# Optimization experiments

Measured on AMD Instinct MI355X. Metric: run time of the kernel, lower is better.

## Reference

```python
import jax, jax.numpy as jnp
import numpy as np

B, S, DIN, H, DOUT, E, SEL = 8, 2048, 512, 512, 512, 262144, 512
N = B * S


def setup_inputs() -> dict:
    key = jax.random.key(0)
    ks = jax.random.split(key, 20)
    inp = {
        "x": jax.random.normal(ks[0], (B, S, DIN), dtype=jnp.float32),
        "edge_index": jax.random.randint(ks[1], (2, E), 0, N, dtype=jnp.int64),
        "selected_idx": jax.random.randint(ks[2], (B, SEL), 0, S, dtype=jnp.int64),
        "edge_label": jax.random.randint(ks[3], (E,), 0, 8, dtype=jnp.int64),
    }
    k = 4
    for l, fin in enumerate([DIN, H, H]):
        inp[f"conv{l}_w1"] = jax.random.normal(ks[k], (2 * fin, H), dtype=jnp.float32) * 0.02; k += 1
        inp[f"conv{l}_b1"] = jnp.full((H,), 0.01, dtype=jnp.float32)
        inp[f"conv{l}_w2"] = jax.random.normal(ks[k], (H, H), dtype=jnp.float32) * 0.02; k += 1
        inp[f"conv{l}_b2"] = jnp.full((H,), 0.01, dtype=jnp.float32)
    inp["ffn_w1"] = jax.random.normal(ks[k], (H, H), dtype=jnp.float32) * 0.02; k += 1
    inp["ffn_b1"] = jnp.full((H,), 0.01, dtype=jnp.float32)
    inp["ffn_w2"] = jax.random.normal(ks[k], (H, DOUT), dtype=jnp.float32) * 0.02; k += 1
    inp["ffn_b2"] = jnp.full((DOUT,), 0.01, dtype=jnp.float32)
    return inp


def _ffw(x, w1, b1, w2, b2):
    # FeedForward: fc2(act_dropout(relu(fc1(x)))), dropout=0 in eval
    return jax.nn.relu(x @ w1 + b1) @ w2 + b2


def reference(x, edge_index, selected_idx, edge_label,
              conv0_w1, conv0_b1, conv0_w2, conv0_b2,
              conv1_w1, conv1_b1, conv1_w2, conv1_b2,
              conv2_w1, conv2_b1, conv2_w2, conv2_b2,
              ffn_w1, ffn_b1, ffn_w2, ffn_b2):
    b, s, d = x.shape
    n = b * s
    h = x.reshape(n, d)
    src, dst = edge_index[0], edge_index[1]  # PyG: x_j = source, x_i = target
    convs = [(conv0_w1, conv0_b1, conv0_w2, conv0_b2),
             (conv1_w1, conv1_b1, conv1_w2, conv1_b2),
             (conv2_w1, conv2_b1, conv2_w2, conv2_b2)]
    for w1, b1, w2, b2 in convs:
        xi = h[dst]                                   # [E, F]
        xj = h[src]
        ef = jnp.concatenate([xi, xj - xi], axis=1)   # [E, 2F]
        m = _ffw(ef, w1, b1, w2, b2)                  # per-edge MLP [E, H]
        agg = jax.ops.segment_max(m, dst, num_segments=n)
        agg = jnp.where(jnp.isneginf(agg), 0.0, agg)  # empty segments -> 0 (PyG fill)
        h = jax.nn.relu(agg)                          # dropout p acts as identity in eval
    h = _ffw(h, ffn_w1, ffn_b1, ffn_w2, ffn_b2)
    out = h.reshape(b, s, -1)                         # [B, S, DOUT]
    idx = jnp.broadcast_to(selected_idx[:, :, None], (b, selected_idx.shape[1], out.shape[-1]))
    return jnp.take_along_axis(out, idx, axis=1)      # [B, SEL, DOUT]
```

## Files before the change

### kernel.cpp

```cpp
#include <hip/hip_runtime.h>
#include <hip/hip_bf16.h>


#define N_NODES 16384
#define EDGES   262144
#define HDIM    512
#define SEQ     2048

typedef __attribute__((ext_vector_type(8))) short short8;
typedef __attribute__((ext_vector_type(8))) _Float16 half8;
typedef __attribute__((ext_vector_type(2))) _Float16 half2v;
typedef __attribute__((ext_vector_type(4))) float f32x4;

__device__ __forceinline__ void gld16(const void* g, void* l) {
    __builtin_amdgcn_global_load_lds(
        (const __attribute__((address_space(1))) void*)g,
        (__attribute__((address_space(3))) void*)l, 16, 0, 0);
}
__device__ __forceinline__ unsigned short f2b(float f) {
    unsigned int x = __float_as_uint(f);
    return (unsigned short)((x + 0x7fffu + ((x >> 16) & 1u)) >> 16);
}
__device__ __forceinline__ unsigned short f2h(float f) {
    _Float16 h = (_Float16)f;
    return __builtin_bit_cast(unsigned short, h);
}
__device__ __forceinline__ unsigned int zpack_h(unsigned int u, unsigned int v) {
    half2v a = __builtin_bit_cast(half2v, u);
    half2v b = __builtin_bit_cast(half2v, v);
    half2v s = a + b;
    half2v z = {(_Float16)0.f, (_Float16)0.f};
    half2v r = __builtin_elementwise_max(s, z);
    return __builtin_bit_cast(unsigned int, r);
}
__device__ __forceinline__ short8 frag_ld(const short* S, int row, int q) {
    int p = q ^ ((row >> 1) & 3);
    return *(const short8*)(S + row * 32 + p * 8);
}
__device__ __forceinline__ void stage_tile(const short* G, int kc, short* S, int t) {
#pragma unroll
    for (int it = 0; it < 2; ++it) {
        int lin = it * 256 + t;
        int row = lin >> 2, p = lin & 3;
        int q = p ^ ((row >> 1) & 3);
        gld16(G + (size_t)row * HDIM + kc + q * 8, S + lin * 8);
    }
}
__device__ __forceinline__ half8 frag64(const short* S, int row, int q) {
    int p = q ^ ((row >> 1) & 7) ^ (row & 1);
    return *(const half8*)(S + row * 64 + p * 8);
}

__global__ __launch_bounds__(256) void hist_kernel(
    const int* __restrict__ dst, int* __restrict__ hist) {
    int idx = blockIdx.x * 256 + threadIdx.x;
    atomicAdd(&hist[dst[idx]], 1);
}
__global__ __launch_bounds__(256) void scan_kernel(
    const int* __restrict__ hist, int* __restrict__ cursor) {
    __shared__ int part[256];
    const int t = threadIdx.x, base = t * 64;
    int sum = 0;
    for (int i = 0; i < 64; ++i) sum += hist[base + i];
    part[t] = sum;
    __syncthreads();
    int run = 0;
    for (int i = 0; i < t; ++i) run += part[i];
    for (int i = 0; i < 64; ++i) {
        int h = hist[base + i];
        cursor[base + i] = run;
        run += h;
    }
}
__global__ __launch_bounds__(256) void scatter_kernel(
    const int* __restrict__ dst, const int* __restrict__ src,
    int* __restrict__ cursor, int* __restrict__ dstS, int* __restrict__ srcS) {
    int idx = blockIdx.x * 256 + threadIdx.x;
    int d = dst[idx];
    int p = atomicAdd(&cursor[d], 1);
    dstS[p] = d;
    srcS[p] = src[idx];
}

__global__ __launch_bounds__(256) void prep_weights_all_kernel(
    const float* __restrict__ w1_0, const float* __restrict__ w2_0,
    const float* __restrict__ w1_1, const float* __restrict__ w2_1,
    const float* __restrict__ w1_2, const float* __restrict__ w2_2,
    short* __restrict__ outbase) {
    __shared__ float tile[32][33];
    const int z = blockIdx.z;
    const int layer = z / 3, which = z % 3;
    const float* w1 = layer == 0 ? w1_0 : (layer == 1 ? w1_1 : w1_2);
    const float* w2 = layer == 0 ? w2_0 : (layer == 1 ? w2_1 : w2_2);
    const int k0 = blockIdx.x * 32, n0 = blockIdx.y * 32;
    const int tx = threadIdx.x, ty = threadIdx.y;
#pragma unroll
    for (int i = 0; i < 4; ++i) {
        int k = k0 + ty + i * 8, n = n0 + tx;
        float v;
        if (which == 0)      v = w1[k * 512 + n] - w1[(k + 512) * 512 + n];
        else if (which == 1) v = w1[(k + 512) * 512 + n];
        else                 v = w2[k * 512 + n];
        tile[ty + i * 8][tx] = v;
    }
    __syncthreads();
    short* out = outbase + (size_t)(layer * 3 + which) * 512 * 512;
#pragma unroll
    for (int i = 0; i < 4; ++i) {
        int n = n0 + ty + i * 8, k = k0 + tx;
        float v = tile[tx][ty + i * 8];
        int lane = (n & 15) | (((k >> 3) & 3) << 4);
        size_t idx = ((size_t)((n >> 4) * 16 + (k >> 5)) * 64 + lane) * 8 + (k & 7);
        out[idx] = (short)(which == 2 ? f2h(v) : f2b(v));
    }
}
__global__ __launch_bounds__(256) void tr_kernel(
    const float* __restrict__ W1, const float* __restrict__ W2,
    short* __restrict__ T1, short* __restrict__ T2) {
    __shared__ float tile[32][33];
    const float* W = blockIdx.z ? W2 : W1;
    short* T = blockIdx.z ? T2 : T1;
    const int k0 = blockIdx.x * 32, n0 = blockIdx.y * 32;
    const int tx = threadIdx.x, ty = threadIdx.y;
#pragma unroll
    for (int i = 0; i < 4; ++i)
        tile[ty + i * 8][tx] = W[(k0 + ty + i * 8) * 512 + n0 + tx];
    __syncthreads();
#pragma unroll
    for (int i = 0; i < 4; ++i)
        T[(size_t)(n0 + ty + i * 8) * 512 + k0 + tx] = (short)f2b(tile[tx][ty + i * 8]);
}
__global__ __launch_bounds__(256) void cvt_bf16_kernel(
    const float* __restrict__ x, short* __restrict__ xb) {
    int idx = blockIdx.x * 256 + threadIdx.x;
    float4 v = ((const float4*)x)[idx];
    uint2 o;
    o.x = (unsigned int)f2b(v.x) | ((unsigned int)f2b(v.y) << 16);
    o.y = (unsigned int)f2b(v.z) | ((unsigned int)f2b(v.w) << 16);
    ((uint2*)xb)[idx] = o;
}

__global__ __launch_bounds__(256, 2) void node_gemm_uv_kernel(
    const short* __restrict__ A, const short* __restrict__ WdF,
    const short* __restrict__ w1bF, const float* __restrict__ b1,
    short* __restrict__ U, short* __restrict__ V) {
    __shared__ short As[2][128 * 32];
    const int t = threadIdx.x;
    const int m0 = blockIdx.x * 128, n0 = blockIdx.y * 128;
    const int w = t >> 6, l = t & 63;
    const int wm = (w & 1) * 64, wn = (w >> 1) * 64;
    const short* Ag = A + (size_t)m0 * HDIM;
    const short* bpU = WdF + (size_t)((n0 + wn) >> 4) * 8192 + (size_t)l * 8;
    const short* bpV = w1bF + (size_t)((n0 + wn) >> 4) * 8192 + (size_t)l * 8;
    f32x4 aU[4][4] = {}, aV[4][4] = {};
    short8 bu2[2][4], bv2[2][4];
    stage_tile(Ag, 0, As[0], t);
#pragma unroll
    for (int nt = 0; nt < 4; ++nt) bu2[0][nt] = *(const short8*)(bpU + nt * 8192);
#pragma unroll
    for (int nt = 0; nt < 4; ++nt) bv2[0][nt] = *(const short8*)(bpV + nt * 8192);
    asm volatile("s_waitcnt vmcnt(8)" ::: "memory");
    __builtin_amdgcn_s_barrier();
    asm volatile("" ::: "memory");
#pragma unroll
    for (int hh = 0; hh < 16; ++hh) {
        short8 a[4];
#pragma unroll
        for (int mt = 0; mt < 4; ++mt)
            a[mt] = frag_ld(As[hh & 1], wm + mt * 16 + (l & 15), l >> 4);
        if (hh < 15) {
#pragma unroll
            for (int nt = 0; nt < 4; ++nt)
                bu2[(hh + 1) & 1][nt] = *(const short8*)(bpU + nt * 8192 + (hh + 1) * 512);
            stage_tile(Ag, (hh + 1) * 32, As[(hh + 1) & 1], t);
            asm volatile("" ::: "memory");
        }
        __builtin_amdgcn_s_setprio(1);
#pragma unroll
        for (int mt = 0; mt < 4; ++mt)
#pragma unroll
            for (int nt = 0; nt < 4; ++nt)
                aU[mt][nt] = __builtin_amdgcn_mfma_f32_16x16x32_bf16(a[mt], bu2[hh & 1][nt], aU[mt][nt], 0, 0, 0);
        __builtin_amdgcn_s_setprio(0);
        if (hh < 15) {
#pragma unroll
            for (int nt = 0; nt < 4; ++nt)
                bv2[(hh + 1) & 1][nt] = *(const short8*)(bpV + nt * 8192 + (hh + 1) * 512);
        }
        __builtin_amdgcn_s_setprio(1);
#pragma unroll
        for (int mt = 0; mt < 4; ++mt)
#pragma unroll
            for (int nt = 0; nt < 4; ++nt)
                aV[mt][nt] = __builtin_amdgcn_mfma_f32_16x16x32_bf16(a[mt], bv2[hh & 1][nt], aV[mt][nt], 0, 0, 0);
        __builtin_amdgcn_s_setprio(0);
        if (hh < 15) {
            asm volatile("s_waitcnt vmcnt(4) lgkmcnt(0)" ::: "memory");
            __builtin_amdgcn_s_barrier();
            asm volatile("" ::: "memory");
        }
    }
#pragma unroll
    for (int mt = 0; mt < 4; ++mt) {
        int m = m0 + wm + mt * 16 + (l >> 4) * 4;
#pragma unroll
        for (int nt = 0; nt < 4; ++nt) {
            int n = n0 + wn + nt * 16 + (l & 15);
            float bv = b1[n];
#pragma unroll
            for (int r = 0; r < 4; ++r) {
                U[(size_t)(m + r) * HDIM + n] = (short)f2h(aU[mt][nt][r] + bv);
                V[(size_t)(m + r) * HDIM + n] = (short)f2h(aV[mt][nt][r]);
            }
        }
    }
}

__device__ __forceinline__ unsigned int fkey(float m) {
    unsigned int b = __float_as_uint(m);
    return ((int)b < 0) ? ~b : (b | 0x80000000u);
}
__device__ __forceinline__ void kflush(unsigned int* K, int d, int col, float m) {
    atomicMax(K + (((size_t)d) << 9) + col, fkey(m));
}
__global__ __launch_bounds__(256, 3) void edge_mfma_kernel(
    const short* __restrict__ U, const short* __restrict__ V,
    const short* __restrict__ W2f, const int* __restrict__ srcS,
    const int* __restrict__ dstS, unsigned int* __restrict__ K) {
    __shared__ short As[64 * 64];
    __shared__ unsigned int ktile[16 * 256];
    __shared__ int sdst[64], ssrc[64];
    const int t = threadIdx.x;
    const int L  = blockIdx.x;
    const int g  = (L >> 4) * 8 + (L & 7);
    const int nh = (L >> 3) & 1;
    const int e0 = g * 64, n0 = nh * 256;
    if (t < 64) { sdst[t] = dstS[e0 + t]; ssrc[t] = srcS[e0 + t]; }
    __syncthreads();
    const int w = t >> 6, l = t & 63;
    const int wnb = w * 64;
    const int lm = l & 15;
    const int arow = t >> 2, s0 = (t & 3) * 2;
    const int perm = ((arow >> 1) & 7) ^ (arow & 1);
    const int p0 = s0 ^ perm, p1 = (s0 + 1) ^ perm;
    const short* up = U + (((size_t)sdst[arow]) << 9) + s0 * 8;
    const short* vp = V + (((size_t)ssrc[arow]) << 9) + s0 * 8;
    const short* bp = W2f + (size_t)((n0 + wnb) >> 4) * 8192 + (size_t)l * 8;
    unsigned int* As_u = (unsigned int*)As;
    f32x4 acc[4][4] = {};
    half8 bc[4], bn[4];
    uint4 pu0, pu1, pv0, pv1;
#pragma unroll
    for (int nt = 0; nt < 4; ++nt) bc[nt] = *(const half8*)(bp + nt * 8192);
    pu0 = *(const uint4*)(up);      pu1 = *(const uint4*)(up + 8);
    pv0 = *(const uint4*)(vp);      pv1 = *(const uint4*)(vp + 8);
    {
        uint4 z0, z1;
        z0.x = zpack_h(pu0.x, pv0.x); z0.y = zpack_h(pu0.y, pv0.y);
        z0.z = zpack_h(pu0.z, pv0.z); z0.w = zpack_h(pu0.w, pv0.w);
        z1.x = zpack_h(pu1.x, pv1.x); z1.y = zpack_h(pu1.y, pv1.y);
        z1.z = zpack_h(pu1.z, pv1.z); z1.w = zpack_h(pu1.w, pv1.w);
        *(uint4*)(As_u + arow * 32 + p0 * 4) = z0;
        *(uint4*)(As_u + arow * 32 + p1 * 4) = z1;
    }
    pu0 = *(const uint4*)(up + 64); pu1 = *(const uint4*)(up + 72);
    pv0 = *(const uint4*)(vp + 64); pv1 = *(const uint4*)(vp + 72);
    asm volatile("s_waitcnt lgkmcnt(0)" ::: "memory");
    __builtin_amdgcn_s_barrier();
    asm volatile("" ::: "memory");
#pragma unroll
    for (int j = 0; j < 8; ++j) {
        const int h1 = 2 * j + 1;
#pragma unroll
        for (int nt = 0; nt < 4; ++nt)
            bn[nt] = *(const half8*)(bp + nt * 8192 + h1 * 512);
        __builtin_amdgcn_s_setprio(1);
#pragma unroll
        for (int mt = 0; mt < 4; ++mt) {
            half8 a = frag64(As, mt * 16 + lm, (l >> 4));
#pragma unroll
            for (int nt = 0; nt < 4; ++nt)
                acc[mt][nt] = __builtin_amdgcn_mfma_f32_16x16x32_f16(a, bc[nt], acc[mt][nt], 0, 0, 0);
        }
        __builtin_amdgcn_s_setprio(0);
        if (j < 7) {
#pragma unroll
            for (int nt = 0; nt < 4; ++nt)
                bc[nt] = *(const half8*)(bp + nt * 8192 + (h1 + 1) * 512);
        }
        __builtin_amdgcn_s_setprio(1);
#pragma unroll
        for (int mt = 0; mt < 4; ++mt) {
            half8 a = frag64(As, mt * 16 + lm, 4 + (l >> 4));
#pragma unroll
            for (int nt = 0; nt < 4; ++nt)
                acc[mt][nt] = __builtin_amdgcn_mfma_f32_16x16x32_f16(a, bn[nt], acc[mt][nt], 0, 0, 0);
        }
        __builtin_amdgcn_s_setprio(0);
        asm volatile("s_waitcnt lgkmcnt(0)" ::: "memory");
        __builtin_amdgcn_s_barrier();
        asm volatile("" ::: "memory");
        if (j < 7) {
            uint4 z0, z1;
            z0.x = zpack_h(pu0.x, pv0.x); z0.y = zpack_h(pu0.y, pv0.y);
            z0.z = zpack_h(pu0.z, pv0.z); z0.w = zpack_h(pu0.w, pv0.w);
            z1.x = zpack_h(pu1.x, pv1.x); z1.y = zpack_h(pu1.y, pv1.y);
            z1.z = zpack_h(pu1.z, pv1.z); z1.w = zpack_h(pu1.w, pv1.w);
            *(uint4*)(As_u + arow * 32 + p0 * 4) = z0;
            *(uint4*)(As_u + arow * 32 + p1 * 4) = z1;
            if (j < 6) {
                const int kn = (j + 2) * 64;
                pu0 = *(const uint4*)(up + kn);      pu1 = *(const uint4*)(up + kn + 8);
                pv0 = *(const uint4*)(vp + kn);      pv1 = *(const uint4*)(vp + kn + 8);
            }
            asm volatile("s_waitcnt lgkmcnt(0)" ::: "memory");
            __builtin_amdgcn_s_barrier();
            asm volatile("" ::: "memory");
        }
    }
    const int dbase = sdst[0];
    const int drange = sdst[63] - dbase + 1;
    if (drange <= 16) {
#pragma unroll
        for (int i = 0; i < 16; ++i) ktile[i * 256 + t] = 0u;
        __syncthreads();
#pragma unroll
        for (int mt = 0; mt < 4; ++mt) {
            int base = mt * 16 + (l >> 4) * 4;
            int d0 = sdst[base], d1 = sdst[base + 1], d2 = sdst[base + 2], d3 = sdst[base + 3];
            int r0 = d0 - dbase, r1 = d1 - dbase, r2 = d2 - dbase, r3 = d3 - dbase;
#pragma unroll
            for (int nt = 0; nt < 4; ++nt) {
                int colb = wnb + nt * 16 + lm;
                f32x4 a = acc[mt][nt];
                float m = a[0];
                if (d1 == d0) m = fmaxf(m, a[1]);
                else { atomicMax(ktile + r0 * 256 + colb, fkey(m)); m = a[1]; }
                if (d2 == d1) m = fmaxf(m, a[2]);
                else { atomicMax(ktile + r1 * 256 + colb, fkey(m)); m = a[2]; }
                if (d3 == d2) m = fmaxf(m, a[3]);
                else { atomicMax(ktile + r2 * 256 + colb, fkey(m)); m = a[3]; }
                atomicMax(ktile + r3 * 256 + colb, fkey(m));
            }
        }
        __syncthreads();
#pragma unroll 4
        for (int r = 0; r < 16; ++r) {
            if (r < drange) {
                unsigned int kv = ktile[r * 256 + t];
                if (kv) atomicMax(K + (((size_t)(dbase + r)) << 9) + n0 + t, kv);
            }
        }
    } else {
#pragma unroll
        for (int mt = 0; mt < 4; ++mt) {
            int base = mt * 16 + (l >> 4) * 4;
            int d0 = sdst[base], d1 = sdst[base + 1], d2 = sdst[base + 2], d3 = sdst[base + 3];
#pragma unroll
            for (int nt = 0; nt < 4; ++nt) {
                int col = n0 + wnb + nt * 16 + lm;
                f32x4 a = acc[mt][nt];
                float m = a[0];
                if (d1 == d0) m = fmaxf(m, a[1]); else { kflush(K, d0, col, m); m = a[1]; }
                if (d2 == d1) m = fmaxf(m, a[2]); else { kflush(K, d1, col, m); m = a[2]; }
                if (d3 == d2) m = fmaxf(m, a[3]); else { kflush(K, d2, col, m); m = a[3]; }
                kflush(K, d3, col, m);
            }
        }
    }
}

__global__ __launch_bounds__(256) void decode_kernel(
    unsigned int* __restrict__ K, const float* __restrict__ b2,
    short* __restrict__ hb) {
    int idx = blockIdx.x * 256 + threadIdx.x;
    uint2 k = ((uint2*)K)[idx];
    uint2 zz = {0u, 0u};
    ((uint2*)K)[idx] = zz;
    int c = (idx << 1) & (HDIM - 1);
    float v0 = 0.f, v1 = 0.f;
    if (k.x != 0u) {
        unsigned int b = (k.x & 0x80000000u) ? (k.x ^ 0x80000000u) : ~k.x;
        v0 = __uint_as_float(b) + b2[c];
    }
    if (k.y != 0u) {
        unsigned int b = (k.y & 0x80000000u) ? (k.y ^ 0x80000000u) : ~k.y;
        v1 = __uint_as_float(b) + b2[c + 1];
    }
    unsigned int o = (unsigned int)f2b(fmaxf(v0, 0.f))
                   | ((unsigned int)f2b(fmaxf(v1, 0.f)) << 16);
    ((unsigned int*)hb)[idx] = o;
}

__global__ __launch_bounds__(256) void ffn_gemm_kernel(
    const short* __restrict__ A, const int* __restrict__ sel,
    const short* __restrict__ Wt, const float* __restrict__ bias,
    short* __restrict__ Cb, float* __restrict__ Cf, int relu) {
    __shared__ short As[64 * 32];
    __shared__ short Bs[128 * 32];
    const int t = threadIdx.x;
    const int m0 = blockIdx.x * 64, n0 = blockIdx.y * 128;
    const int w = t >> 6, l = t & 63;
    const int wm = (w & 1) * 32, wn = (w >> 1) * 64;
    const int srow = t >> 2, sp = t & 3;
    const int sq = sp ^ ((srow >> 1) & 3);
    const short* ap;
    if (sel) {
        int gr = m0 + srow;
        ap = A + (((size_t)((gr >> 9) * SEQ + sel[gr])) << 9);
    } else {
        ap = A + (size_t)(m0 + srow) * HDIM;
    }
    f32x4 acc[2][4] = {};
    for (int kc = 0; kc < HDIM; kc += 32) {
        gld16(ap + kc + sq * 8, As + t * 8);
        stage_tile(Wt + (size_t)n0 * HDIM, kc, Bs, t);
        __syncthreads();
        short8 a[2], b[4];
#pragma unroll
        for (int mt = 0; mt < 2; ++mt) a[mt] = frag_ld(As, wm + mt * 16 + (l & 15), l >> 4);
#pragma unroll
        for (int nt = 0; nt < 4; ++nt) b[nt] = frag_ld(Bs, wn + nt * 16 + (l & 15), l >> 4);
#pragma unroll
        for (int mt = 0; mt < 2; ++mt)
#pragma unroll
            for (int nt = 0; nt < 4; ++nt)
                acc[mt][nt] = __builtin_amdgcn_mfma_f32_16x16x32_bf16(a[mt], b[nt], acc[mt][nt], 0, 0, 0);
        __syncthreads();
    }
#pragma unroll
    for (int mt = 0; mt < 2; ++mt) {
        int m = m0 + wm + mt * 16 + (l >> 4) * 4;
#pragma unroll
        for (int nt = 0; nt < 4; ++nt) {
            int n = n0 + wn + nt * 16 + (l & 15);
            float bv = bias[n];
#pragma unroll
            for (int r = 0; r < 4; ++r) {
                float v = acc[mt][nt][r] + bv;
                if (relu) v = fmaxf(v, 0.f);
                if (Cf) Cf[(size_t)(m + r) * HDIM + n] = v;
                else    Cb[(size_t)(m + r) * HDIM + n] = (short)f2b(v);
            }
        }
    }
}

extern "C" void kernel_launch(void* const* d_in, const int* in_sizes, int n_in,
                              void* d_out, int out_size, void* d_ws, size_t ws_size,
                              hipStream_t stream) {
    const float* x   = (const float*)d_in[0];
    const int*   ei  = (const int*)d_in[1];
    const int*   sel = (const int*)d_in[2];
    const int*   src = ei;
    const int*   dst = ei + EDGES;
    const float* cw1[3] = {(const float*)d_in[4],  (const float*)d_in[8],  (const float*)d_in[12]};
    const float* cb1[3] = {(const float*)d_in[5],  (const float*)d_in[9],  (const float*)d_in[13]};
    const float* cw2[3] = {(const float*)d_in[6],  (const float*)d_in[10], (const float*)d_in[14]};
    const float* cb2[3] = {(const float*)d_in[7],  (const float*)d_in[11], (const float*)d_in[15]};
    const float* fw1 = (const float*)d_in[16];
    const float* fb1 = (const float*)d_in[17];
    const float* fw2 = (const float*)d_in[18];
    const float* fb2 = (const float*)d_in[19];
    float* out = (float*)d_out;

    const size_t MB = 1024 * 1024;
    char* p = (char*)d_ws;
    unsigned int* keys = (unsigned int*)p;
    short* U    = (short*)(p + 32 * MB);
    short* V    = (short*)(p + 48 * MB);
    short* hb   = (short*)(p + 64 * MB);
    short* Wall = (short*)(p + 80 * MB);
    short* fw1T = Wall + 9 * 512 * 512;
    short* fw2T = fw1T + 512 * 512;
    int*   dstS = (int*)(p + 86 * MB);
    int*   srcS = (int*)(p + 87 * MB);
    int*   hist = (int*)(p + 88 * MB);
    int*   curs = hist + N_NODES;
    short* t1b  = (short*)(p + 89 * MB);

    (void)hipMemsetAsync(hist, 0, N_NODES * sizeof(int), stream);
    hist_kernel<<<EDGES / 256, 256, 0, stream>>>(dst, hist);
    scan_kernel<<<1, 256, 0, stream>>>(hist, curs);
    scatter_kernel<<<EDGES / 256, 256, 0, stream>>>(dst, src, curs, dstS, srcS);

    cvt_bf16_kernel<<<8192, 256, 0, stream>>>(x, hb);
    tr_kernel<<<dim3(16, 16, 2), dim3(32, 8), 0, stream>>>(fw1, fw2, fw1T, fw2T);
    prep_weights_all_kernel<<<dim3(16, 16, 9), dim3(32, 8), 0, stream>>>(
        cw1[0], cw2[0], cw1[1], cw2[1], cw1[2], cw2[2], Wall);
    (void)hipMemsetAsync(keys, 0, 32 * MB, stream);

    for (int l = 0; l < 3; ++l) {
        short* WdF  = Wall + (size_t)(l * 3 + 0) * 512 * 512;
        short* w1bF = Wall + (size_t)(l * 3 + 1) * 512 * 512;
        short* W2f  = Wall + (size_t)(l * 3 + 2) * 512 * 512;
        node_gemm_uv_kernel<<<dim3(128, 4), 256, 0, stream>>>(hb, WdF, w1bF, cb1[l], U, V);
        edge_mfma_kernel<<<8192, 256, 0, stream>>>(U, V, W2f, srcS, dstS, keys);
        decode_kernel<<<(N_NODES * HDIM / 2) / 256, 256, 0, stream>>>(keys, cb2[l], hb);
    }

    ffn_gemm_kernel<<<dim3(64, 4), 256, 0, stream>>>(hb, sel, fw1T, fb1, t1b, nullptr, 1);
    ffn_gemm_kernel<<<dim3(64, 4), 256, 0, stream>>>(t1b, nullptr, fw2T, fb2, nullptr, out, 0);
}
```

Before: 717.2 us.

## Double-buffer edge A tile in LDS and merge FFN weight transpose into prep kernel

The edge MFMA kernel now keeps two LDS buffers for the packed U/V operand tile. The next chunk is written into the alternate buffer while MFMAs read the current one, which drops one of the two barriers per iteration, and the B-fragment prefetch is moved earlier. The separate FFN weight transpose kernel is folded into the weight prep kernel as two extra z-slices, saving one launch. The cost is 8 KB more LDS per block, which may lower occupancy below the declared three blocks per CU.

```diff
diff --git a/kernel.cpp b/kernel.cpp
--- a/kernel.cpp
+++ b/kernel.cpp
@@ -86,49 +86,46 @@
     const float* __restrict__ w1_0, const float* __restrict__ w2_0,
     const float* __restrict__ w1_1, const float* __restrict__ w2_1,
     const float* __restrict__ w1_2, const float* __restrict__ w2_2,
-    short* __restrict__ outbase) {
+    const float* __restrict__ fw1, const float* __restrict__ fw2,
+    short* __restrict__ outbase, short* __restrict__ fT1, short* __restrict__ fT2) {
     __shared__ float tile[32][33];
     const int z = blockIdx.z;
-    const int layer = z / 3, which = z % 3;
-    const float* w1 = layer == 0 ? w1_0 : (layer == 1 ? w1_1 : w1_2);
-    const float* w2 = layer == 0 ? w2_0 : (layer == 1 ? w2_1 : w2_2);
     const int k0 = blockIdx.x * 32, n0 = blockIdx.y * 32;
     const int tx = threadIdx.x, ty = threadIdx.y;
-#pragma unroll
-    for (int i = 0; i < 4; ++i) {
-        int k = k0 + ty + i * 8, n = n0 + tx;
-        float v;
-        if (which == 0)      v = w1[k * 512 + n] - w1[(k + 512) * 512 + n];
-        else if (which == 1) v = w1[(k + 512) * 512 + n];
-        else                 v = w2[k * 512 + n];
-        tile[ty + i * 8][tx] = v;
-    }
-    __syncthreads();
-    short* out = outbase + (size_t)(layer * 3 + which) * 512 * 512;
-#pragma unroll
-    for (int i = 0; i < 4; ++i) {
-        int n = n0 + ty + i * 8, k = k0 + tx;
-        float v = tile[tx][ty + i * 8];
-        int lane = (n & 15) | (((k >> 3) & 3) << 4);
-        size_t idx = ((size_t)((n >> 4) * 16 + (k >> 5)) * 64 + lane) * 8 + (k & 7);
-        out[idx] = (short)(which == 2 ? f2h(v) : f2b(v));
-    }
-}
-__global__ __launch_bounds__(256) void tr_kernel(
-    const float* __restrict__ W1, const float* __restrict__ W2,
-    short* __restrict__ T1, short* __restrict__ T2) {
-    __shared__ float tile[32][33];
-    const float* W = blockIdx.z ? W2 : W1;
-    short* T = blockIdx.z ? T2 : T1;
-    const int k0 = blockIdx.x * 32, n0 = blockIdx.y * 32;
-    const int tx = threadIdx.x, ty = threadIdx.y;
-#pragma unroll
-    for (int i = 0; i < 4; ++i)
-        tile[ty + i * 8][tx] = W[(k0 + ty + i * 8) * 512 + n0 + tx];
-    __syncthreads();
-#pragma unroll
-    for (int i = 0; i < 4; ++i)
-        T[(size_t)(n0 + ty + i * 8) * 512 + k0 + tx] = (short)f2b(tile[tx][ty + i * 8]);
+    if (z < 9) {
+        const int layer = z / 3, which = z % 3;
+        const float* w1 = layer == 0 ? w1_0 : (layer == 1 ? w1_1 : w1_2);
+        const float* w2 = layer == 0 ? w2_0 : (layer == 1 ? w2_1 : w2_2);
+#pragma unroll
+        for (int i = 0; i < 4; ++i) {
+            int k = k0 + ty + i * 8, n = n0 + tx;
+            float v;
+            if (which == 0)      v = w1[k * 512 + n] - w1[(k + 512) * 512 + n];
+            else if (which == 1) v = w1[(k + 512) * 512 + n];
+            else                 v = w2[k * 512 + n];
+            tile[ty + i * 8][tx] = v;
+        }
+        __syncthreads();
+        short* out = outbase + (size_t)(layer * 3 + which) * 512 * 512;
+#pragma unroll
+        for (int i = 0; i < 4; ++i) {
+            int n = n0 + ty + i * 8, k = k0 + tx;
+            float v = tile[tx][ty + i * 8];
+            int lane = (n & 15) | (((k >> 3) & 3) << 4);
+            size_t idx = ((size_t)((n >> 4) * 16 + (k >> 5)) * 64 + lane) * 8 + (k & 7);
+            out[idx] = (short)(which == 2 ? f2h(v) : f2b(v));
+        }
+    } else {
+        const float* W = (z == 9) ? fw1 : fw2;
+        short* T = (z == 9) ? fT1 : fT2;
+#pragma unroll
+        for (int i = 0; i < 4; ++i)
+            tile[ty + i * 8][tx] = W[(k0 + ty + i * 8) * 512 + n0 + tx];
+        __syncthreads();
+#pragma unroll
+        for (int i = 0; i < 4; ++i)
+            T[(size_t)(n0 + ty + i * 8) * 512 + k0 + tx] = (short)f2b(tile[tx][ty + i * 8]);
+    }
 }
 __global__ __launch_bounds__(256) void cvt_bf16_kernel(
     const float* __restrict__ x, short* __restrict__ xb) {
@@ -227,7 +224,7 @@
     const short* __restrict__ U, const short* __restrict__ V,
     const short* __restrict__ W2f, const int* __restrict__ srcS,
     const int* __restrict__ dstS, unsigned int* __restrict__ K) {
-    __shared__ short As[64 * 64];
+    __shared__ short As[2][64 * 64];
     __shared__ unsigned int ktile[16 * 256];
     __shared__ int sdst[64], ssrc[64];
     const int t = threadIdx.x;
@@ -246,12 +243,13 @@
     const short* up = U + (((size_t)sdst[arow]) << 9) + s0 * 8;
     const short* vp = V + (((size_t)ssrc[arow]) << 9) + s0 * 8;
     const short* bp = W2f + (size_t)((n0 + wnb) >> 4) * 8192 + (size_t)l * 8;
-    unsigned int* As_u = (unsigned int*)As;
     f32x4 acc[4][4] = {};
     half8 bc[4], bn[4];
     uint4 pu0, pu1, pv0, pv1;
 #pragma unroll
     for (int nt = 0; nt < 4; ++nt) bc[nt] = *(const half8*)(bp + nt * 8192);
+#pragma unroll
+    for (int nt = 0; nt < 4; ++nt) bn[nt] = *(const half8*)(bp + nt * 8192 + 512);
     pu0 = *(const uint4*)(up);      pu1 = *(const uint4*)(up + 8);
     pv0 = *(const uint4*)(vp);      pv1 = *(const uint4*)(vp + 8);
     {
@@ -260,8 +258,9 @@
         z0.z = zpack_h(pu0.z, pv0.z); z0.w = zpack_h(pu0.w, pv0.w);
         z1.x = zpack_h(pu1.x, pv1.x); z1.y = zpack_h(pu1.y, pv1.y);
         z1.z = zpack_h(pu1.z, pv1.z); z1.w = zpack_h(pu1.w, pv1.w);
-        *(uint4*)(As_u + arow * 32 + p0 * 4) = z0;
-        *(uint4*)(As_u + arow * 32 + p1 * 4) = z1;
+        unsigned int* du = (unsigned int*)As[0];
+        *(uint4*)(du + arow * 32 + p0 * 4) = z0;
+        *(uint4*)(du + arow * 32 + p1 * 4) = z1;
     }
     pu0 = *(const uint4*)(up + 64); pu1 = *(const uint4*)(up + 72);
     pv0 = *(const uint4*)(vp + 64); pv1 = *(const uint4*)(vp + 72);
@@ -270,14 +269,11 @@
     asm volatile("" ::: "memory");
 #pragma unroll
     for (int j = 0; j < 8; ++j) {
-        const int h1 = 2 * j + 1;
-#pragma unroll
-        for (int nt = 0; nt < 4; ++nt)
-            bn[nt] = *(const half8*)(bp + nt * 8192 + h1 * 512);
+        const short* Ab = As[j & 1];
         __builtin_amdgcn_s_setprio(1);
 #pragma unroll
         for (int mt = 0; mt < 4; ++mt) {
-            half8 a = frag64(As, mt * 16 + lm, (l >> 4));
+            half8 a = frag64(Ab, mt * 16 + lm, (l >> 4));
 #pragma unroll
             for (int nt = 0; nt < 4; ++nt)
                 acc[mt][nt] = __builtin_amdgcn_mfma_f32_16x16x32_f16(a, bc[nt], acc[mt][nt], 0, 0, 0);
@@ -286,37 +282,38 @@
         if (j < 7) {
 #pragma unroll
             for (int nt = 0; nt < 4; ++nt)
-                bc[nt] = *(const half8*)(bp + nt * 8192 + (h1 + 1) * 512);
+                bc[nt] = *(const half8*)(bp + nt * 8192 + (2 * j + 2) * 512);
         }
         __builtin_amdgcn_s_setprio(1);
 #pragma unroll
         for (int mt = 0; mt < 4; ++mt) {
-            half8 a = frag64(As, mt * 16 + lm, 4 + (l >> 4));
+            half8 a = frag64(Ab, mt * 16 + lm, 4 + (l >> 4));
 #pragma unroll
             for (int nt = 0; nt < 4; ++nt)
                 acc[mt][nt] = __builtin_amdgcn_mfma_f32_16x16x32_f16(a, bn[nt], acc[mt][nt], 0, 0, 0);
         }
         __builtin_amdgcn_s_setprio(0);
-        asm volatile("s_waitcnt lgkmcnt(0)" ::: "memory");
-        __builtin_amdgcn_s_barrier();
-        asm volatile("" ::: "memory");
         if (j < 7) {
+#pragma unroll
+            for (int nt = 0; nt < 4; ++nt)
+                bn[nt] = *(const half8*)(bp + nt * 8192 + (2 * j + 3) * 512);
             uint4 z0, z1;
             z0.x = zpack_h(pu0.x, pv0.x); z0.y = zpack_h(pu0.y, pv0.y);
             z0.z = zpack_h(pu0.z, pv0.z); z0.w = zpack_h(pu0.w, pv0.w);
             z1.x = zpack_h(pu1.x, pv1.x); z1.y = zpack_h(pu1.y, pv1.y);
             z1.z = zpack_h(pu1.z, pv1.z); z1.w = zpack_h(pu1.w, pv1.w);
-            *(uint4*)(As_u + arow * 32 + p0 * 4) = z0;
-            *(uint4*)(As_u + arow * 32 + p1 * 4) = z1;
+            unsigned int* du = (unsigned int*)As[(j + 1) & 1];
+            *(uint4*)(du + arow * 32 + p0 * 4) = z0;
+            *(uint4*)(du + arow * 32 + p1 * 4) = z1;
             if (j < 6) {
                 const int kn = (j + 2) * 64;
                 pu0 = *(const uint4*)(up + kn);      pu1 = *(const uint4*)(up + kn + 8);
                 pv0 = *(const uint4*)(vp + kn);      pv1 = *(const uint4*)(vp + kn + 8);
             }
-            asm volatile("s_waitcnt lgkmcnt(0)" ::: "memory");
-            __builtin_amdgcn_s_barrier();
-            asm volatile("" ::: "memory");
-        }
+        }
+        asm volatile("s_waitcnt lgkmcnt(0)" ::: "memory");
+        __builtin_amdgcn_s_barrier();
+        asm volatile("" ::: "memory");
     }
     const int dbase = sdst[0];
     const int drange = sdst[63] - dbase + 1;
@@ -485,9 +482,8 @@
     scatter_kernel<<<EDGES / 256, 256, 0, stream>>>(dst, src, curs, dstS, srcS);
 
     cvt_bf16_kernel<<<8192, 256, 0, stream>>>(x, hb);
-    tr_kernel<<<dim3(16, 16, 2), dim3(32, 8), 0, stream>>>(fw1, fw2, fw1T, fw2T);
-    prep_weights_all_kernel<<<dim3(16, 16, 9), dim3(32, 8), 0, stream>>>(
-        cw1[0], cw2[0], cw1[1], cw2[1], cw1[2], cw2[2], Wall);
+    prep_weights_all_kernel<<<dim3(16, 16, 11), dim3(32, 8), 0, stream>>>(
+        cw1[0], cw2[0], cw1[1], cw2[1], cw1[2], cw2[2], fw1, fw2, Wall, fw1T, fw2T);
     (void)hipMemsetAsync(keys, 0, 32 * MB, stream);
 
     for (int l = 0; l < 3; ++l) {
```

Measured after the change: 717.1 us. About the same (-0.0%).
